# Kernel optimization log

Measured on AMD Instinct MI355X. Metric: run time of the kernel, lower is better.

Reference implementation:

```python
import jax, jax.numpy as jnp
import numpy as np

N = 200000
E = 600000
H = 128
OUT = 256
NUM_TYPES = 300
B = 128


def setup_inputs() -> dict:
    key = jax.random.key(0)
    ks = jax.random.split(key, 12)
    x = jax.random.randint(ks[0], (N,), 0, NUM_TYPES)
    edge_index = jax.random.randint(ks[1], (2, E), 0, N)
    batch = jnp.sort(jax.random.randint(ks[2], (N,), 0, B))
    s = 1.0 / np.sqrt(H)
    emb = jax.random.normal(ks[3], (NUM_TYPES, H), jnp.float32)
    W0 = jax.random.uniform(ks[4], (H, H), jnp.float32, -s, s)
    b0 = jax.random.uniform(ks[5], (H,), jnp.float32, -s, s)
    W1 = jax.random.uniform(ks[6], (H, H), jnp.float32, -s, s)
    b1 = jax.random.uniform(ks[7], (H,), jnp.float32, -s, s)
    Wo = jax.random.uniform(ks[8], (H, OUT), jnp.float32, -s, s)
    bo = jax.random.uniform(ks[9], (OUT,), jnp.float32, -s, s)
    gamma = jnp.ones((OUT,), jnp.float32)
    beta = jnp.zeros((OUT,), jnp.float32)
    return {"x": x, "edge_index": edge_index, "batch": batch, "batch_size": B,
            "emb": emb, "W0": W0, "b0": b0, "W1": W1, "b1": b1,
            "Wo": Wo, "bo": bo, "gamma": gamma, "beta": beta}


def gcn_layer(h, full_src, full_dst, W, b, n):
    # gather messages, scatter-add to destinations (bidirectional edges pre-built)
    msg = h[full_src]                                   # [2E, H]
    agg = jax.ops.segment_sum(msg, full_dst, num_segments=n)
    deg = jax.ops.segment_sum(jnp.ones((full_src.shape[0],), h.dtype),
                              full_dst, num_segments=n)
    deg = jnp.sqrt(jnp.clip(deg, 1.0))[:, None]
    out = agg / deg
    out = out @ W + b
    out = out + h
    return jax.nn.gelu(out, approximate=False)  # torch nn.GELU default is exact


def reference(x, edge_index, batch, batch_size, emb, W0, b0, W1, b1, Wo, bo, gamma, beta):
    n = x.shape[0]
    h = emb[x]                                          # [N, H] embedding gather
    src, dst = edge_index[0], edge_index[1]
    full_src = jnp.concatenate([src, dst])
    full_dst = jnp.concatenate([dst, src])
    h = gcn_layer(h, full_src, full_dst, W0, b0, n)
    h = gcn_layer(h, full_src, full_dst, W1, b1, n)
    # segment-mean pooling per graph
    gsum = jax.ops.segment_sum(h, batch, num_segments=batch_size)
    cnt = jax.ops.segment_sum(jnp.ones((n,), h.dtype), batch, num_segments=batch_size)
    gfeat = gsum / jnp.clip(cnt, 1.0)[:, None]
    out = gfeat @ Wo + bo
    mu = jnp.mean(out, axis=-1, keepdims=True)
    var = jnp.var(out, axis=-1, keepdims=True)
    out = (out - mu) * jax.lax.rsqrt(var + 1e-5) * gamma + beta
    return out
```

## Files before the change

kernel.cpp:

```cpp
#include <hip/hip_runtime.h>
#include <hip/hip_bf16.h>
#include <hip/hip_fp8.h>
#include <math.h>

#define H 128
#define OUTD 256
#define ASTRIDE 40
#define NODE_MASK 0x3FFFF
#define EPAD 144
#define EMB_LDS_MAX 38400

typedef unsigned short ushort_t;
typedef unsigned int uint_t;
typedef unsigned char uchar_t;
typedef __attribute__((ext_vector_type(8))) short short8;
typedef __attribute__((ext_vector_type(4))) float f32x4;
typedef __attribute__((ext_vector_type(2))) float f32x2;

__device__ __forceinline__ float bf2f(uint_t u){
    union { uint_t i; float f; } v; v.i = u << 16; return v.f;
}
__device__ __forceinline__ uint_t f2bf(float f){
    __hip_bfloat16 b = __float2bfloat16(f);
    union { __hip_bfloat16 b; ushort_t u; } v; v.b = b; return (uint_t)v.u;
}
__device__ __forceinline__ float fp8tof(uint_t u){
    __hip_fp8_e4m3 t; t.__x = (__hip_fp8_storage_t)u; return (float)t;
}
__device__ __forceinline__ uint_t ftofp8(float f){
    __hip_fp8_e4m3 t(f); return (uint_t)t.__x;
}
__device__ __forceinline__ uint_t pk2fp8(float a, float b){
#if __has_builtin(__builtin_amdgcn_cvt_pk_fp8_f32)
    return (uint_t)__builtin_amdgcn_cvt_pk_fp8_f32(a, b, 0, false) & 0xFFFFu;
#else
    return ftofp8(a) | (ftofp8(b) << 8);
#endif
}
__device__ __forceinline__ void acc_fp8(f32x4& v, uint_t u){
#if __has_builtin(__builtin_amdgcn_cvt_pk_f32_fp8)
    f32x2 lo = __builtin_amdgcn_cvt_pk_f32_fp8(u, false);
    f32x2 hi = __builtin_amdgcn_cvt_pk_f32_fp8(u, true);
    f32x2 a = {v[0], v[1]}, b2 = {v[2], v[3]};
    a += lo; b2 += hi;
    v = (f32x4){a[0], a[1], b2[0], b2[1]};
#else
    v[0] += fp8tof(u & 0xFFu);         v[1] += fp8tof((u >> 8) & 0xFFu);
    v[2] += fp8tof((u >> 16) & 0xFFu); v[3] += fp8tof(u >> 24);
#endif
}
__device__ __forceinline__ float gelu_fast(float x){
    float a = fabsf(x) * 0.70710678118654752440f;
    float t = __builtin_amdgcn_rcpf(fmaf(0.3275911f, a, 1.0f));
    float p = t*fmaf(t, fmaf(t, fmaf(t, fmaf(t, 1.061405429f, -1.453152027f),
                                     1.421413741f), -0.284496736f), 0.254829592f);
    float erf = 1.0f - p*__expf(-a*a);
    erf = copysignf(erf, x);
    return 0.5f * x * (1.0f + erf);
}

__global__ __launch_bounds__(256) void sniff_part(const ushort_t* __restrict__ data,
                                                  int count, float* __restrict__ partial){
    __shared__ float red[256];
    float m = 0.f;
    for (int i = blockIdx.x*256 + threadIdx.x; i < count; i += gridDim.x*256){
        float v = fabsf(bf2f((uint_t)data[i]));
        if (isfinite(v)) m = fmaxf(m, v);
        else m = 1e30f;
    }
    red[threadIdx.x] = m;
    __syncthreads();
    #pragma unroll
    for (int s = 128; s > 0; s >>= 1){
        if (threadIdx.x < s) red[threadIdx.x] = fmaxf(red[threadIdx.x], red[threadIdx.x+s]);
        __syncthreads();
    }
    if (threadIdx.x == 0) partial[blockIdx.x] = red[0];
}
__global__ __launch_bounds__(64) void sniff_fin(const float* __restrict__ partial,
                                                int nb, int* __restrict__ flag_fp32){
    if (threadIdx.x == 0){
        float m = 0.f;
        for (int i = 0; i < nb; i++) m = fmaxf(m, partial[i]);
        *flag_fp32 = (m > 100.f) ? 1 : 0;
    }
}

struct StageArgs {
    const void* src[7];
    float*      dst[7];
    int         count[7];
    int         blk_off[8];
};
__global__ __launch_bounds__(256) void stage_all_kernel(StageArgs args,
                                                        const int* __restrict__ flag_fp32){
    int bx = blockIdx.x;
    int seg = 0;
    while (seg < 6 && bx >= args.blk_off[seg+1]) seg++;
    int idx = (bx - args.blk_off[seg])*256 + threadIdx.x;
    if (idx >= args.count[seg]) return;
    const int isf32 = *flag_fp32;
    args.dst[seg][idx] = isf32 ? ((const float*)args.src[seg])[idx]
                               : bf2f((uint_t)((const ushort_t*)args.src[seg])[idx]);
}

__global__ __launch_bounds__(256) void transpose_w_kernel(
        const void* __restrict__ Ws0, const void* __restrict__ Ws1,
        const void* __restrict__ embsrc, int szEmb,
        ushort_t* __restrict__ d0, ushort_t* __restrict__ d1,
        ushort_t* __restrict__ dEmb, uchar_t* __restrict__ dEmb8,
        int* __restrict__ zero_base, int zero_count,
        const int* __restrict__ flag_fp32){
    if (blockIdx.y == 3){
        for (int i = blockIdx.x*256 + threadIdx.x; i < zero_count; i += gridDim.x*256)
            zero_base[i] = 0;
        return;
    }
    const int isf32 = *flag_fp32;
    if (blockIdx.y == 2){
        int i = blockIdx.x*256 + threadIdx.x;
        if (i >= szEmb) return;
        ushort_t bv = isf32 ? (ushort_t)f2bf(((const float*)embsrc)[i])
                            : ((const ushort_t*)embsrc)[i];
        dEmb[i] = bv;
        int row = i >> 7, col = i & 127;
        int kb = col >> 5, qq = (col >> 3) & 3, jj = col & 7;
        dEmb8[(size_t)row*H + qq*32 + kb*8 + jj] = (uchar_t)ftofp8(bf2f((uint_t)bv));
        return;
    }
    const void* s = blockIdx.y ? Ws1 : Ws0;
    ushort_t*   d = blockIdx.y ? d1  : d0;
    int i = blockIdx.x*256 + threadIdx.x;
    if (i >= H*H) return;
    int k = i >> 7, nn = i & 127;
    ushort_t v = isf32 ? (ushort_t)f2bf(((const float*)s)[i])
                       : ((const ushort_t*)s)[i];
    d[nn*H + k] = v;
}

__global__ __launch_bounds__(256) void fill_part_kernel(const int* __restrict__ src,
        const int* __restrict__ dst, const int* __restrict__ x,
        int* __restrict__ deg, int* __restrict__ adj, int E, int n){
    int group = blockIdx.x & 7;
    int gblk  = blockIdx.x >> 3;
    int G     = gridDim.x >> 3;
    int lo = (int)(((long long)n * group) / 8);
    int hi = (int)(((long long)n * (group+1)) / 8);
    for (int e = gblk*256 + threadIdx.x; e < E; e += G*256){
        int s = src[e], d = dst[e];
        if (d >= lo && d < hi){
            int ts = x[s];
            int p = atomicAdd(&deg[d], 1);
            if (p < ASTRIDE) adj[(size_t)d*ASTRIDE + p] = s | (ts << 18);
        }
        if (s >= lo && s < hi){
            int td = x[d];
            int p = atomicAdd(&deg[s], 1);
            if (p < ASTRIDE) adj[(size_t)s*ASTRIDE + p] = d | (td << 18);
        }
    }
}

#define L1STEP(EV) do { if (jcur < cnt){ \
    uint_t t_ = (EV) >> 18; \
    const uchar_t* hp_ = &Es[t_*EPAD + quad*32]; \
    uint4 r0_ = *(const uint4*)(hp_); \
    uint4 r1_ = *(const uint4*)(hp_ + 16); \
    acc_fp8(g[0], r0_.x); acc_fp8(g[1], r0_.y); \
    acc_fp8(g[2], r0_.z); acc_fp8(g[3], r0_.w); \
    acc_fp8(g[4], r1_.x); acc_fp8(g[5], r1_.y); \
    acc_fp8(g[6], r1_.z); acc_fp8(g[7], r1_.w); } jcur++; } while(0)

template<int MODE>
__global__ __launch_bounds__(512, 6) void gcn_fused(
    const int* __restrict__ deg, const int* __restrict__ adj,
    const ushort_t* __restrict__ gsrc, const uchar_t* __restrict__ g8,
    const int* __restrict__ xmap,
    const ushort_t* __restrict__ WT, const float* __restrict__ b,
    ushort_t* __restrict__ h_out, uchar_t* __restrict__ h8_out,
    int n, int szEmb){
    __shared__ ushort_t Wt[128*136];
    __shared__ uchar_t Es[(MODE == 1) ? 300*EPAD : 16];
    for (int i = threadIdx.x; i < 2048; i += 512){
        int nn = i >> 4;
        int k0 = (i & 15) << 3;
        *(uint4*)(&Wt[nn*136 + k0]) = *(const uint4*)(WT + nn*H + k0);
    }
    if (MODE == 1){
        const uint4* esrc = (const uint4*)g8;
        int nq = szEmb >> 4;
        for (int i = threadIdx.x; i < nq; i += 512){
            int r = i >> 3, c = i & 7;
            *(uint4*)(&Es[r*EPAD + c*16]) = esrc[i];
        }
    }
    __syncthreads();
    const int lane = threadIdx.x & 63;
    const int wave = threadIdx.x >> 6;
    const int quad = lane >> 4;
    const int lid  = lane & 15;

    int row = blockIdx.x*128 + wave*16 + lid;
    int cnt = (row < n) ? deg[row] : 0;
    float s = rsqrtf((float)(cnt < 1 ? 1 : cnt));
    if (cnt > ASTRIDE) cnt = ASTRIDE;
    const uint_t* ap = (const uint_t*)(adj + (size_t)row*ASTRIDE);

    f32x4 g[8];
    #pragma unroll
    for (int i=0;i<8;i++) g[i] = (f32x4){0.f,0.f,0.f,0.f};

    if (MODE == 1){
        const uint4* ap4 = (const uint4*)ap;
        uint4 ew0 = {0,0,0,0}, ew1 = {0,0,0,0}, ew2 = {0,0,0,0};
        if (row < n){ ew0 = ap4[0]; ew1 = ap4[1]; ew2 = ap4[2]; }
        int jcur = 0;
        L1STEP(ew0.x); L1STEP(ew0.y); L1STEP(ew0.z); L1STEP(ew0.w);
        L1STEP(ew1.x); L1STEP(ew1.y); L1STEP(ew1.z); L1STEP(ew1.w);
        L1STEP(ew2.x); L1STEP(ew2.y); L1STEP(ew2.z); L1STEP(ew2.w);
        for (int j = 12; j < cnt; j++){
            uint_t t = ap[j] >> 18;
            const uchar_t* hp = &Es[t*EPAD + quad*32];
            uint4 r0 = *(const uint4*)(hp);
            uint4 r1 = *(const uint4*)(hp + 16);
            acc_fp8(g[0], r0.x); acc_fp8(g[1], r0.y);
            acc_fp8(g[2], r0.z); acc_fp8(g[3], r0.w);
            acc_fp8(g[4], r1.x); acc_fp8(g[5], r1.y);
            acc_fp8(g[6], r1.z); acc_fp8(g[7], r1.w);
        }
    } else {
        uint4 c0 = {0,0,0,0}, c1 = {0,0,0,0}, n0 = {0,0,0,0}, n1 = {0,0,0,0};
        if (cnt > 0){
            uint_t e = ap[0];
            size_t ro = (size_t)(MODE ? (e >> 18) : (e & NODE_MASK)) * H;
            const uchar_t* hp = g8 + ro + quad*32;
            c0 = *(const uint4*)(hp); c1 = *(const uint4*)(hp + 16);
        }
        if (cnt > 1){
            uint_t e = ap[1];
            size_t ro = (size_t)(MODE ? (e >> 18) : (e & NODE_MASK)) * H;
            const uchar_t* hp = g8 + ro + quad*32;
            n0 = *(const uint4*)(hp); n1 = *(const uint4*)(hp + 16);
        }
        for (int j=0; j<cnt; j++){
            uint4 f0 = {0,0,0,0}, f1 = {0,0,0,0};
            if (j+2 < cnt){
                uint_t e = ap[j+2];
                size_t ro = (size_t)(MODE ? (e >> 18) : (e & NODE_MASK)) * H;
                const uchar_t* hp = g8 + ro + quad*32;
                f0 = *(const uint4*)(hp); f1 = *(const uint4*)(hp + 16);
            }
            acc_fp8(g[0], c0.x); acc_fp8(g[1], c0.y);
            acc_fp8(g[2], c0.z); acc_fp8(g[3], c0.w);
            acc_fp8(g[4], c1.x); acc_fp8(g[5], c1.y);
            acc_fp8(g[6], c1.z); acc_fp8(g[7], c1.w);
            c0 = n0; c1 = n1; n0 = f0; n1 = f1;
        }
    }

    short8 afrag[4];
    #pragma unroll
    for (int kb=0;kb<4;kb++){
        uint_t w0 = f2bf(g[2*kb][0]*s)   | (f2bf(g[2*kb][1]*s)   << 16);
        uint_t w1 = f2bf(g[2*kb][2]*s)   | (f2bf(g[2*kb][3]*s)   << 16);
        uint_t w2 = f2bf(g[2*kb+1][0]*s) | (f2bf(g[2*kb+1][1]*s) << 16);
        uint_t w3 = f2bf(g[2*kb+1][2]*s) | (f2bf(g[2*kb+1][3]*s) << 16);
        uint4 packed; packed.x=w0; packed.y=w1; packed.z=w2; packed.w=w3;
        afrag[kb] = *(short8*)&packed;
    }

    f32x4 acc[8];
    #pragma unroll
    for (int ct=0;ct<8;ct++) acc[ct] = (f32x4){0.f,0.f,0.f,0.f};
    #pragma unroll
    for (int kb=0;kb<4;kb++){
        #pragma unroll
        for (int ct=0;ct<8;ct++){
            short8 bf = *(const short8*)(&Wt[(ct*16+lid)*136 + kb*32 + quad*8]);
            acc[ct] = __builtin_amdgcn_mfma_f32_16x16x32_bf16(afrag[kb], bf, acc[ct], 0,0,0);
        }
    }

    float bcol[8];
    #pragma unroll
    for (int ct=0;ct<8;ct++) bcol[ct] = b[ct*16 + lid];
    int rowq = blockIdx.x*128 + wave*16 + quad*4;
    bool full = (blockIdx.x*128 + wave*16 + 16) <= n;
    const int boff = ((lid >> 3) << 5) + (lid & 7);
    #pragma unroll
    for (int r=0;r<4;r++){
        int grow = rowq + r;
        if (full || grow < n){
            if (MODE != 0){
                const ushort_t* hr = gsrc + (size_t)xmap[grow]*H + lid;
                uchar_t* o8 = h8_out + (size_t)grow*H;
                float vv[8];
                #pragma unroll
                for (int ct=0;ct<8;ct++){
                    float hv = bf2f((uint_t)hr[ct*16]);
                    vv[ct] = gelu_fast(acc[ct][r] + bcol[ct] + hv);
                }
                #pragma unroll
                for (int cp=0;cp<4;cp++){
                    uint_t pk = pk2fp8(vv[2*cp], vv[2*cp+1]);
                    o8[boff + cp*8]      = (uchar_t)(pk & 0xFF);
                    o8[boff + 64 + cp*8] = (uchar_t)(pk >> 8);
                }
            } else {
                const uchar_t* h8r = g8 + (size_t)grow*H;
                ushort_t* orp = h_out + (size_t)grow*H + lid;
                #pragma unroll
                for (int ct=0;ct<8;ct++){
                    int off2 = boff + ((ct & 1) << 6) + ((ct >> 1) << 3);
                    float hv = fp8tof((uint_t)h8r[off2]);
                    float v  = gelu_fast(acc[ct][r] + bcol[ct] + hv);
                    orp[ct*16] = (ushort_t)f2bf(v);
                }
            }
        }
    }
}

__global__ __launch_bounds__(256) void pool_kernel(const ushort_t* __restrict__ h,
        const int* __restrict__ batch, float* __restrict__ gfeat, int n){
    int g = blockIdx.x;
    int q = blockIdx.y;
    __shared__ int se[2];
    if (threadIdx.x == 0){
        int lo=0, hi=n;
        while (lo<hi){ int m=(lo+hi)>>1; if (batch[m] < g) lo=m+1; else hi=m; }
        se[0] = lo;
        hi = n;
        while (lo<hi){ int m=(lo+hi)>>1; if (batch[m] <= g) lo=m+1; else hi=m; }
        se[1] = lo;
    }
    __syncthreads();
    int start = se[0], end = se[1];
    int chunk = (end - start + 3) >> 2;
    int s = start + q*chunk;
    int e = s + chunk; if (e > end) e = end;
    int col0 = (threadIdx.x & 15) << 3;
    int rg   = threadIdx.x >> 4;
    float acc[8];
    #pragma unroll
    for (int i=0;i<8;i++) acc[i] = 0.f;
    for (int r = s + rg; r < e; r += 16){
        uint4 raw = *(const uint4*)(h + (size_t)r*H + col0);
        acc[0] += bf2f(raw.x & 0xFFFFu); acc[1] += bf2f(raw.x >> 16);
        acc[2] += bf2f(raw.y & 0xFFFFu); acc[3] += bf2f(raw.y >> 16);
        acc[4] += bf2f(raw.z & 0xFFFFu); acc[5] += bf2f(raw.z >> 16);
        acc[6] += bf2f(raw.w & 0xFFFFu); acc[7] += bf2f(raw.w >> 16);
    }
    __shared__ float red[16][128];
    #pragma unroll
    for (int i=0;i<8;i++) red[rg][col0+i] = acc[i];
    __syncthreads();
    #pragma unroll
    for (int st=8; st>=1; st>>=1){
        if (rg < st){
            #pragma unroll
            for (int i=0;i<8;i++) red[rg][col0+i] += red[rg+st][col0+i];
        }
        __syncthreads();
    }
    if (rg == 0){
        #pragma unroll
        for (int i=0;i<8;i++) atomicAdd(&gfeat[(size_t)g*H + col0 + i], red[0][col0+i]);
    }
}

__global__ __launch_bounds__(256) void head_kernel(const float* __restrict__ gfeat,
        const int* __restrict__ batch, int n,
        const float* __restrict__ Wo, const float* __restrict__ bo,
        const float* __restrict__ gamma, const float* __restrict__ beta,
        void* __restrict__ out, const int* __restrict__ flag_fp32){
    int g = blockIdx.x;
    int j = threadIdx.x;
    __shared__ float gf[H];
    __shared__ float icnt_sh;
    if (j == 0){
        int lo=0, hi=n;
        while (lo<hi){ int m=(lo+hi)>>1; if (batch[m] < g) lo=m+1; else hi=m; }
        int st = lo;
        hi = n;
        while (lo<hi){ int m=(lo+hi)>>1; if (batch[m] <= g) lo=m+1; else hi=m; }
        int cnt = lo - st; if (cnt < 1) cnt = 1;
        icnt_sh = 1.0f / (float)cnt;
    }
    __syncthreads();
    if (j < H) gf[j] = gfeat[(size_t)g*H + j] * icnt_sh;
    __syncthreads();
    float acc = bo[j];
    #pragma unroll 8
    for (int k=0;k<H;k++) acc += gf[k] * Wo[(size_t)k*OUTD + j];
    __shared__ float red[256];
    red[j] = acc;
    __syncthreads();
    #pragma unroll
    for (int s2=128;s2>0;s2>>=1){
        if (j < s2) red[j] += red[j+s2];
        __syncthreads();
    }
    float mu = red[0] * (1.f/OUTD);
    __syncthreads();
    float d = acc - mu;
    red[j] = d*d;
    __syncthreads();
    #pragma unroll
    for (int s2=128;s2>0;s2>>=1){
        if (j < s2) red[j] += red[j+s2];
        __syncthreads();
    }
    float var = red[0] * (1.f/OUTD);
    float val = d * rsqrtf(var + 1e-5f) * gamma[j] + beta[j];
    size_t idx = (size_t)g*OUTD + j;
    if (*flag_fp32) ((float*)out)[idx] = val;
    else            ((ushort_t*)out)[idx] = (ushort_t)f2bf(val);
}

extern "C" void kernel_launch(void* const* d_in, const int* in_sizes, int n_in,
                              void* d_out, int out_size, void* d_ws, size_t ws_size,
                              hipStream_t stream){
    const int* x     = (const int*)d_in[0];
    const int* edge  = (const int*)d_in[1];
    const int* batch = (const int*)d_in[2];

    const int n = in_sizes[0];
    const int E = in_sizes[1] / 2;
    const int B = out_size / OUTD;
    const int* srcp = edge;
    const int* dstp = edge + E;

    const int szEmb = in_sizes[4], szb0 = in_sizes[6], szb1 = in_sizes[8];
    const int szWo = in_sizes[9], szbo = in_sizes[10], szg = in_sizes[11], szbt = in_sizes[12];

    char* base = (char*)d_ws;
    size_t off = 0;
    auto take = [&](size_t bytes)->char*{
        char* p = base + off;
        off = (off + bytes + 15) & ~(size_t)15;
        return p;
    };
    int*   flag   = (int*)  take(4);
    float* spart  = (float*)take(64*4);
    ushort_t* embb= (ushort_t*)take((size_t)szEmb*2);
    uchar_t* emb8 = (uchar_t*)take((size_t)szEmb);
    ushort_t* WT0 = (ushort_t*)take((size_t)H*H*2);
    ushort_t* WT1 = (ushort_t*)take((size_t)H*H*2);
    float* sb0    = (float*)take((size_t)szb0*4);
    float* sb1    = (float*)take((size_t)szb1*4);
    float* sWo    = (float*)take((size_t)szWo*4);
    float* sbo    = (float*)take((size_t)szbo*4);
    float* sg     = (float*)take((size_t)szg*4);
    float* sbt    = (float*)take((size_t)szbt*4);
    int*   adj    = (int*)  take((size_t)n*ASTRIDE*4);
    ushort_t* hA  = (ushort_t*)take((size_t)n*H*2);
    uchar_t*  h8  = (uchar_t*)take((size_t)n*H);
    char* zbase   = take((size_t)n*4 + (size_t)B*H*4);
    int*   deg    = (int*)zbase;
    float* gfeat  = (float*)(zbase + (size_t)n*4);
    const int zero_ints = n + B*H;

    sniff_part<<<64, 256, 0, stream>>>((const ushort_t*)d_in[4], szEmb, spart);
    sniff_fin<<<1, 64, 0, stream>>>(spart, 64, flag);

    StageArgs sa;
    const void* ssrc[7] = {d_in[9], d_in[6], d_in[8], d_in[10], d_in[11], d_in[12], d_in[10]};
    float*      sdst[7] = {sWo, sb0, sb1, sbo, sg, sbt, sbo};
    int         scnt[7] = {szWo, szb0, szb1, szbo, szg, szbt, 0};
    int run = 0;
    for (int i=0;i<7;i++){
        sa.src[i] = ssrc[i]; sa.dst[i] = sdst[i]; sa.count[i] = scnt[i];
        sa.blk_off[i] = run; run += (scnt[i] + 255)/256;
    }
    sa.blk_off[7] = run;
    stage_all_kernel<<<run, 256, 0, stream>>>(sa, flag);
    int tgrid = ((H*H > szEmb ? H*H : szEmb) + 255)/256;
    transpose_w_kernel<<<dim3(tgrid, 4), 256, 0, stream>>>(d_in[5], d_in[7],
                                                           d_in[4], szEmb,
                                                           WT0, WT1, embb, emb8,
                                                           (int*)zbase, zero_ints, flag);

    fill_part_kernel<<<2048, 256, 0, stream>>>(srcp, dstp, x, deg, adj, E, n);

    const int nblk = (n + 127) / 128;
    if (szEmb <= EMB_LDS_MAX)
        gcn_fused<1><<<nblk, 512, 0, stream>>>(deg, adj, embb, emb8, x,
                                               WT0, sb0, (ushort_t*)nullptr, h8,
                                               n, szEmb);
    else
        gcn_fused<2><<<nblk, 512, 0, stream>>>(deg, adj, embb, emb8, x,
                                               WT0, sb0, (ushort_t*)nullptr, h8,
                                               n, szEmb);
    gcn_fused<0><<<nblk, 512, 0, stream>>>(deg, adj, embb, h8, x,
                                           WT1, sb1, hA, (uchar_t*)nullptr,
                                           n, szEmb);

    pool_kernel<<<dim3(B,4), 256, 0, stream>>>(hA, batch, gfeat, n);
    head_kernel<<<B, 256, 0, stream>>>(gfeat, batch, n, sWo, sbo, sg, sbt, d_out, flag);
}
```

Baseline: 301.1 us.

## Fuse graph mean-pool sum into second GCN layer epilogue via atomics

The second GCN layer no longer writes the bf16 node features to global memory. Its epilogue reduces each 16-row stripe across lanes and atomically adds the result into the per-graph sums, which removes the separate pool kernel and the large hA buffer (N×128 bf16 written and then read back). Stripes whose rows span more than one graph fall back to per-row atomics. This adds float atomics into a small 128×128 buffer, with possible contention and a summation order that is no longer deterministic. The L1STEP macro is also rewritten as an unrolled loop, which does not change behaviour.

```diff
diff --git a/kernel.cpp b/kernel.cpp
--- a/kernel.cpp
+++ b/kernel.cpp
@@ -161,23 +161,14 @@
     }
 }
 
-#define L1STEP(EV) do { if (jcur < cnt){ \
-    uint_t t_ = (EV) >> 18; \
-    const uchar_t* hp_ = &Es[t_*EPAD + quad*32]; \
-    uint4 r0_ = *(const uint4*)(hp_); \
-    uint4 r1_ = *(const uint4*)(hp_ + 16); \
-    acc_fp8(g[0], r0_.x); acc_fp8(g[1], r0_.y); \
-    acc_fp8(g[2], r0_.z); acc_fp8(g[3], r0_.w); \
-    acc_fp8(g[4], r1_.x); acc_fp8(g[5], r1_.y); \
-    acc_fp8(g[6], r1_.z); acc_fp8(g[7], r1_.w); } jcur++; } while(0)
-
 template<int MODE>
 __global__ __launch_bounds__(512, 6) void gcn_fused(
     const int* __restrict__ deg, const int* __restrict__ adj,
     const ushort_t* __restrict__ gsrc, const uchar_t* __restrict__ g8,
     const int* __restrict__ xmap,
     const ushort_t* __restrict__ WT, const float* __restrict__ b,
-    ushort_t* __restrict__ h_out, uchar_t* __restrict__ h8_out,
+    uchar_t* __restrict__ h8_out,
+    const int* __restrict__ batchp, float* __restrict__ gfeat,
     int n, int szEmb){
     __shared__ ushort_t Wt[128*136];
     __shared__ uchar_t Es[(MODE == 1) ? 300*EPAD : 16];
@@ -215,9 +206,22 @@
         uint4 ew0 = {0,0,0,0}, ew1 = {0,0,0,0}, ew2 = {0,0,0,0};
         if (row < n){ ew0 = ap4[0]; ew1 = ap4[1]; ew2 = ap4[2]; }
         int jcur = 0;
-        L1STEP(ew0.x); L1STEP(ew0.y); L1STEP(ew0.z); L1STEP(ew0.w);
-        L1STEP(ew1.x); L1STEP(ew1.y); L1STEP(ew1.z); L1STEP(ew1.w);
-        L1STEP(ew2.x); L1STEP(ew2.y); L1STEP(ew2.z); L1STEP(ew2.w);
+        uint_t ews[12] = {ew0.x, ew0.y, ew0.z, ew0.w, ew1.x, ew1.y,
+                          ew1.z, ew1.w, ew2.x, ew2.y, ew2.z, ew2.w};
+        #pragma unroll
+        for (int jj=0; jj<12; jj++){
+            if (jcur < cnt){
+                uint_t t = ews[jj] >> 18;
+                const uchar_t* hp = &Es[t*EPAD + quad*32];
+                uint4 r0 = *(const uint4*)(hp);
+                uint4 r1 = *(const uint4*)(hp + 16);
+                acc_fp8(g[0], r0.x); acc_fp8(g[1], r0.y);
+                acc_fp8(g[2], r0.z); acc_fp8(g[3], r0.w);
+                acc_fp8(g[4], r1.x); acc_fp8(g[5], r1.y);
+                acc_fp8(g[6], r1.z); acc_fp8(g[7], r1.w);
+            }
+            jcur++;
+        }
         for (int j = 12; j < cnt; j++){
             uint_t t = ap[j] >> 18;
             const uchar_t* hp = &Es[t*EPAD + quad*32];
@@ -285,13 +289,14 @@
     #pragma unroll
     for (int ct=0;ct<8;ct++) bcol[ct] = b[ct*16 + lid];
     int rowq = blockIdx.x*128 + wave*16 + quad*4;
-    bool full = (blockIdx.x*128 + wave*16 + 16) <= n;
     const int boff = ((lid >> 3) << 5) + (lid & 7);
-    #pragma unroll
-    for (int r=0;r<4;r++){
-        int grow = rowq + r;
-        if (full || grow < n){
-            if (MODE != 0){
+
+    if (MODE != 0){
+        bool full = (blockIdx.x*128 + wave*16 + 16) <= n;
+        #pragma unroll
+        for (int r=0;r<4;r++){
+            int grow = rowq + r;
+            if (full || grow < n){
                 const ushort_t* hr = gsrc + (size_t)xmap[grow]*H + lid;
                 uchar_t* o8 = h8_out + (size_t)grow*H;
                 float vv[8];
@@ -306,66 +311,46 @@
                     o8[boff + cp*8]      = (uchar_t)(pk & 0xFF);
                     o8[boff + 64 + cp*8] = (uchar_t)(pk >> 8);
                 }
-            } else {
-                const uchar_t* h8r = g8 + (size_t)grow*H;
-                ushort_t* orp = h_out + (size_t)grow*H + lid;
+            }
+        }
+    } else {
+        int stripe = blockIdx.x*128 + wave*16;
+        int i0 = stripe < n ? stripe : (n-1);
+        int i1 = (stripe+15) < n ? (stripe+15) : (n-1);
+        int g0 = batchp[i0];
+        bool fast = ((stripe + 16) <= n) && (g0 == batchp[i1]);
+        if (fast){
+            #pragma unroll
+            for (int ct=0;ct<8;ct++){
+                int off2 = boff + ((ct & 1) << 6) + ((ct >> 1) << 3);
+                float vsum = 0.f;
                 #pragma unroll
-                for (int ct=0;ct<8;ct++){
-                    int off2 = boff + ((ct & 1) << 6) + ((ct >> 1) << 3);
-                    float hv = fp8tof((uint_t)h8r[off2]);
-                    float v  = gelu_fast(acc[ct][r] + bcol[ct] + hv);
-                    orp[ct*16] = (ushort_t)f2bf(v);
+                for (int r=0;r<4;r++){
+                    int grow = rowq + r;
+                    float hv = fp8tof((uint_t)g8[(size_t)grow*H + off2]);
+                    vsum += gelu_fast(acc[ct][r] + bcol[ct] + hv);
+                }
+                vsum += __shfl_xor(vsum, 16);
+                vsum += __shfl_xor(vsum, 32);
+                if (quad == 0)
+                    atomicAdd(&gfeat[(size_t)g0*H + ct*16 + lid], vsum);
+            }
+        } else {
+            #pragma unroll
+            for (int r=0;r<4;r++){
+                int grow = rowq + r;
+                if (grow < n){
+                    int gbid = batchp[grow];
+                    #pragma unroll
+                    for (int ct=0;ct<8;ct++){
+                        int off2 = boff + ((ct & 1) << 6) + ((ct >> 1) << 3);
+                        float hv = fp8tof((uint_t)g8[(size_t)grow*H + off2]);
+                        float v  = gelu_fast(acc[ct][r] + bcol[ct] + hv);
+                        atomicAdd(&gfeat[(size_t)gbid*H + ct*16 + lid], v);
+                    }
                 }
             }
         }
-    }
-}
-
-__global__ __launch_bounds__(256) void pool_kernel(const ushort_t* __restrict__ h,
-        const int* __restrict__ batch, float* __restrict__ gfeat, int n){
-    int g = blockIdx.x;
-    int q = blockIdx.y;
-    __shared__ int se[2];
-    if (threadIdx.x == 0){
-        int lo=0, hi=n;
-        while (lo<hi){ int m=(lo+hi)>>1; if (batch[m] < g) lo=m+1; else hi=m; }
-        se[0] = lo;
-        hi = n;
-        while (lo<hi){ int m=(lo+hi)>>1; if (batch[m] <= g) lo=m+1; else hi=m; }
-        se[1] = lo;
-    }
-    __syncthreads();
-    int start = se[0], end = se[1];
-    int chunk = (end - start + 3) >> 2;
-    int s = start + q*chunk;
-    int e = s + chunk; if (e > end) e = end;
-    int col0 = (threadIdx.x & 15) << 3;
-    int rg   = threadIdx.x >> 4;
-    float acc[8];
-    #pragma unroll
-    for (int i=0;i<8;i++) acc[i] = 0.f;
-    for (int r = s + rg; r < e; r += 16){
-        uint4 raw = *(const uint4*)(h + (size_t)r*H + col0);
-        acc[0] += bf2f(raw.x & 0xFFFFu); acc[1] += bf2f(raw.x >> 16);
-        acc[2] += bf2f(raw.y & 0xFFFFu); acc[3] += bf2f(raw.y >> 16);
-        acc[4] += bf2f(raw.z & 0xFFFFu); acc[5] += bf2f(raw.z >> 16);
-        acc[6] += bf2f(raw.w & 0xFFFFu); acc[7] += bf2f(raw.w >> 16);
-    }
-    __shared__ float red[16][128];
-    #pragma unroll
-    for (int i=0;i<8;i++) red[rg][col0+i] = acc[i];
-    __syncthreads();
-    #pragma unroll
-    for (int st=8; st>=1; st>>=1){
-        if (rg < st){
-            #pragma unroll
-            for (int i=0;i<8;i++) red[rg][col0+i] += red[rg+st][col0+i];
-        }
-        __syncthreads();
-    }
-    if (rg == 0){
-        #pragma unroll
-        for (int i=0;i<8;i++) atomicAdd(&gfeat[(size_t)g*H + col0 + i], red[0][col0+i]);
     }
 }
 
@@ -454,7 +439,6 @@
     float* sg     = (float*)take((size_t)szg*4);
     float* sbt    = (float*)take((size_t)szbt*4);
     int*   adj    = (int*)  take((size_t)n*ASTRIDE*4);
-    ushort_t* hA  = (ushort_t*)take((size_t)n*H*2);
     uchar_t*  h8  = (uchar_t*)take((size_t)n*H);
     char* zbase   = take((size_t)n*4 + (size_t)B*H*4);
     int*   deg    = (int*)zbase;
@@ -486,16 +470,17 @@
     const int nblk = (n + 127) / 128;
     if (szEmb <= EMB_LDS_MAX)
         gcn_fused<1><<<nblk, 512, 0, stream>>>(deg, adj, embb, emb8, x,
-                                               WT0, sb0, (ushort_t*)nullptr, h8,
+                                               WT0, sb0, h8,
+                                               (const int*)nullptr, (float*)nullptr,
                                                n, szEmb);
     else
         gcn_fused<2><<<nblk, 512, 0, stream>>>(deg, adj, embb, emb8, x,
-                                               WT0, sb0, (ushort_t*)nullptr, h8,
+                                               WT0, sb0, h8,
+                                               (const int*)nullptr, (float*)nullptr,
                                                n, szEmb);
     gcn_fused<0><<<nblk, 512, 0, stream>>>(deg, adj, embb, h8, x,
-                                           WT1, sb1, hA, (uchar_t*)nullptr,
-                                           n, szEmb);
-
-    pool_kernel<<<dim3(B,4), 256, 0, stream>>>(hA, batch, gfeat, n);
+                                           WT1, sb1, (uchar_t*)nullptr,
+                                           batch, gfeat, n, szEmb);
+
     head_kernel<<<B, 256, 0, stream>>>(gfeat, batch, n, sWo, sbo, sg, sbt, d_out, flag);
 }
```

Measured after the change: 288.4 us. 4.2% less time.
